# Optimization experiments

Hardware: AMD Instinct MI355X
Metric: run time of the kernel (lower is better)

## Reference

```python
import jax, jax.numpy as jnp
import numpy as np

N = 40000          # spots (nodes)
G = 3000           # genes (input features)
C = 20             # num_classes
E = N * 16         # edges (avg degree 16)


def _uniform(key, shape, stdv):
    return jax.random.uniform(key, shape, jnp.float32, -stdv, stdv)


def _linear_params(key, n_in, n_out):
    # torch Linear default init: U(-1/sqrt(in), 1/sqrt(in)); stored as [in, out]
    k1, k2 = jax.random.split(key)
    s = 1.0 / np.sqrt(n_in)
    return _uniform(k1, (n_in, n_out), s), _uniform(k2, (n_out,), s)


def setup_inputs() -> dict:
    key = jax.random.key(0)
    ks = jax.random.split(key, 32)
    x = jax.random.normal(ks[0], (N, G), jnp.float32)
    adj_rows = jax.random.randint(ks[1], (E,), 0, N, jnp.int32)
    adj_cols = jax.random.randint(ks[2], (E,), 0, N, jnp.int32)
    adj_vals = jax.random.uniform(ks[3], (E,), jnp.float32)

    # GCN weights: GraphConvolution init U(-1/sqrt(out), 1/sqrt(out)), no bias
    def gcn_w(k, fi, fo):
        return _uniform(k, (fi, fo), 1.0 / np.sqrt(fo))

    inp = {
        "x": x, "adj_rows": adj_rows, "adj_cols": adj_cols, "adj_vals": adj_vals,
        "W1": gcn_w(ks[4], G, 512), "W2": gcn_w(ks[5], 512, 256),
        "W3": gcn_w(ks[6], 256, 128), "W4": gcn_w(ks[7], 128, 128),
        "W5": gcn_w(ks[8], 128, C),
    }
    # AE linear layers
    for name, (fi, fo), k in [
        ("enc1", (G, 512), ks[9]), ("enc2", (512, 256), ks[10]),
        ("enc3", (256, 128), ks[11]), ("zl", (128, 128), ks[12]),
        ("dec1", (128, 128), ks[13]), ("dec2", (128, 256), ks[14]),
        ("dec3", (256, 512), ks[15]), ("xbar", (512, G), ks[16]),
    ]:
        w, b = _linear_params(k, fi, fo)
        inp[name + "_w"], inp[name + "_b"] = w, b
    # Attention projection vectors (Linear(in_size, 1, bias=False))
    inp["a1"] = _uniform(ks[17], (512,), 1.0 / np.sqrt(512))
    inp["a2"] = _uniform(ks[18], (256,), 1.0 / np.sqrt(256))
    inp["a3"] = _uniform(ks[19], (128,), 1.0 / np.sqrt(128))
    inp["a4"] = _uniform(ks[20], (128,), 1.0 / np.sqrt(128))
    inp["scale"] = jax.random.normal(ks[21], (G,), jnp.float32)
    inp["additive"] = jax.random.normal(ks[22], (G,), jnp.float32)
    return inp


def _spmm(rows, cols, vals, dense, n):
    # out[r] = sum_e vals[e] * dense[cols[e]] for rows[e]==r  (sparse [n,n] @ dense)
    return jax.ops.segment_sum(vals[:, None] * dense[cols], rows, num_segments=n)


def _gcn(x, rows, cols, vals, W, n, active=True):
    out = _spmm(rows, cols, vals, x @ W, n)
    return jax.nn.relu(out) if active else out


def _attn(h, t, a):
    # stack two [N,D] branches, softmax over the branch axis, weighted sum
    z = jnp.stack([h, t], axis=1)           # [N,2,D]
    w = jnp.einsum('nbd,d->nb', z, a)        # [N,2]
    beta = jax.nn.softmax(w, axis=1)
    return jnp.einsum('nb,nbd->nd', beta, z)


def reference(x, adj_rows, adj_cols, adj_vals,
              W1, W2, W3, W4, W5,
              enc1_w, enc1_b, enc2_w, enc2_b, enc3_w, enc3_b, zl_w, zl_b,
              dec1_w, dec1_b, dec2_w, dec2_b, dec3_w, dec3_b, xbar_w, xbar_b,
              a1, a2, a3, a4, scale, additive):
    n = x.shape[0]
    # autoencoder
    t1 = jax.nn.relu(x @ enc1_w + enc1_b)
    t2 = jax.nn.relu(t1 @ enc2_w + enc2_b)
    t3 = jax.nn.relu(t2 @ enc3_w + enc3_b)
    z = t3 @ zl_w + zl_b
    d1 = jax.nn.relu(z @ dec1_w + dec1_b)
    d2 = jax.nn.relu(d1 @ dec2_w + dec2_b)
    d3 = jax.nn.relu(d2 @ dec3_w + dec3_b)
    x_bar = d3 @ xbar_w + xbar_b
    # GCN stack with attention-fused AE skip connections
    h = _gcn(x, adj_rows, adj_cols, adj_vals, W1, n)
    emb = _attn(h, t1, a1)
    h = _gcn(emb, adj_rows, adj_cols, adj_vals, W2, n)
    emb = _attn(h, t2, a2)
    h = _gcn(emb, adj_rows, adj_cols, adj_vals, W3, n)
    emb = _attn(h, t3, a3)
    h = _gcn(emb, adj_rows, adj_cols, adj_vals, W4, n)
    emb = _attn(h, z, a4)
    output = _gcn(emb, adj_rows, adj_cols, adj_vals, W5, n, active=False)
    return output, x_bar, jax.nn.sigmoid(scale), jnp.exp(additive)
```

## Files before the change

### kernel.cpp

```cpp
#include <hip/hip_runtime.h>
#include <cmath>

typedef unsigned short u16;
typedef unsigned int u32;
typedef __attribute__((ext_vector_type(8))) short short8;
typedef __attribute__((ext_vector_type(4))) short short4v;
typedef __attribute__((ext_vector_type(4))) float f32x4;

__device__ __forceinline__ float bf2f(u16 h) {
  union { u32 u; float f; } v; v.u = ((u32)h) << 16; return v.f;
}
__device__ __forceinline__ u16 f2bf(float f) {
  union { float f; u32 u; } v; v.f = f;
  u32 u = v.u;
  u32 r = (u + 0x7FFFu + ((u >> 16) & 1u)) >> 16;
  return (u16)r;
}

__global__ void convx_kernel(const float* __restrict__ x, u16* __restrict__ A0) {
  int idx = blockIdx.x * 256 + threadIdx.x;
  int r = blockIdx.y;
  if (idx >= 376) return;
  short8 o;
  if (r < 40000 && idx < 375) {
    const float* src = x + (size_t)r * 3000 + idx * 8;
    float4 v0 = *(const float4*)src;
    float4 v1 = *(const float4*)(src + 4);
    o[0] = (short)f2bf(v0.x); o[1] = (short)f2bf(v0.y);
    o[2] = (short)f2bf(v0.z); o[3] = (short)f2bf(v0.w);
    o[4] = (short)f2bf(v1.x); o[5] = (short)f2bf(v1.y);
    o[6] = (short)f2bf(v1.z); o[7] = (short)f2bf(v1.w);
  } else {
#pragma unroll
    for (int j = 0; j < 8; ++j) o[j] = 0;
  }
  *(short8*)(A0 + (size_t)r * 3008 + idx * 8) = o;
}

__global__ void convw_kernel(const float* __restrict__ W, u16* __restrict__ Wt,
                             int K, int N, int Kp) {
  int k = blockIdx.x * 256 + threadIdx.x;
  int n = blockIdx.y;
  if (k >= Kp) return;
  float v = (k < K && n < N) ? W[(size_t)k * N + n] : 0.f;
  Wt[(size_t)n * Kp + k] = f2bf(v);
}

__global__ void zero_kernel(int* p, int n) {
  int i = blockIdx.x * 256 + threadIdx.x;
  if (i < n) p[i] = 0;
}
__global__ void count_kernel(const int* __restrict__ rows, int* __restrict__ counts, int E) {
  int i = blockIdx.x * 256 + threadIdx.x;
  if (i < E) atomicAdd(&counts[rows[i]], 1);
}
__global__ __launch_bounds__(1024) void scan_kernel(const int* __restrict__ counts,
                                                    int* __restrict__ rowptr,
                                                    int* __restrict__ cursor, int n) {
  __shared__ int buf[1024];
  __shared__ int carry_s;
  int tid = threadIdx.x;
  if (tid == 0) carry_s = 0;
  __syncthreads();
  for (int base = 0; base < n; base += 1024) {
    int i = base + tid;
    int v = (i < n) ? counts[i] : 0;
    buf[tid] = v;
    __syncthreads();
    for (int off = 1; off < 1024; off <<= 1) {
      int tv = (tid >= off) ? buf[tid - off] : 0;
      __syncthreads();
      buf[tid] += tv;
      __syncthreads();
    }
    int incl = buf[tid];
    int carry = carry_s;
    if (i < n) { int ex = carry + incl - v; rowptr[i] = ex; cursor[i] = ex; }
    __syncthreads();
    if (tid == 1023) carry_s = carry + incl;
    __syncthreads();
  }
  if (tid == 0) rowptr[n] = carry_s;
}
__global__ void scatter_kernel(const int* __restrict__ rows, const int* __restrict__ cols,
                               const float* __restrict__ vals, int* __restrict__ cursor,
                               int* __restrict__ cols_s, float* __restrict__ vals_s, int E) {
  int i = blockIdx.x * 256 + threadIdx.x;
  if (i < E) {
    int r = rows[i];
    int p = atomicAdd(&cursor[r], 1);
    cols_s[p] = cols[i];
    vals_s[p] = vals[i];
  }
}

#define BM 128
#define BN 128
#define BK 32

template <bool BIAS, bool RELU, bool OUTBF16, int CH>
__global__ __launch_bounds__(256, 2) void gemm_bf16(
    const u16* __restrict__ A, int lda, const u16* __restrict__ Bt, int ldb,
    void* __restrict__ C1, int ldc,
    const float* __restrict__ bias, int M, int Nreal, int K, int MT, int NT) {
  __shared__ __align__(16) u16 As[2][BM * BK];
  __shared__ __align__(16) u16 Bs[2][BN * BK];
  const int lin = blockIdx.x;
  const int per = CH * NT;
  const int g = lin / per;
  const int r0 = lin - g * per;
  const int bx0 = g * CH;
  const int cw = min(CH, MT - bx0);
  const int bx = bx0 + r0 % cw;
  const int by = r0 / cw;

  const int tid = threadIdx.x;
  const int lane = tid & 63;
  const int wave = tid >> 6;
  const int mblk = bx * BM;
  const int nblk = by * BN;
  const int wm = (wave & 1) * 64;
  const int wn = (wave >> 1) * 64;
  const int ml = lane & 15;
  const int kg = lane >> 4;

  f32x4 acc[4][4];
#pragma unroll
  for (int i = 0; i < 4; ++i)
#pragma unroll
    for (int j = 0; j < 4; ++j) acc[i][j] = (f32x4)(0.f);

  const int nk = K / BK;
  const int sr = tid >> 2;
  const int sc = (tid & 3) * 8;
  const u16* gA0 = A + (size_t)(mblk + sr) * lda + sc;
  const u16* gA1 = A + (size_t)(mblk + sr + 64) * lda + sc;
  const u16* gB0 = Bt + (size_t)(nblk + sr) * ldb + sc;
  const u16* gB1 = Bt + (size_t)(nblk + sr + 64) * ldb + sc;

  auto stage = [&](int buf, int kt) {
    const int ko = kt * BK;
    u16* lA = &As[buf][0] + wave * 512;
    u16* lB = &Bs[buf][0] + wave * 512;
    __builtin_amdgcn_global_load_lds((const void*)(gA0 + ko), (void*)lA, 16, 0, 0);
    __builtin_amdgcn_global_load_lds((const void*)(gA1 + ko), (void*)(lA + 2048), 16, 0, 0);
    __builtin_amdgcn_global_load_lds((const void*)(gB0 + ko), (void*)lB, 16, 0, 0);
    __builtin_amdgcn_global_load_lds((const void*)(gB1 + ko), (void*)(lB + 2048), 16, 0, 0);
  };

  stage(0, 0);
  asm volatile("s_waitcnt vmcnt(0)" ::: "memory");
  __syncthreads();

  int cur = 0;
  for (int kt = 0; kt < nk; ++kt) {
    if (kt + 1 < nk) stage(cur ^ 1, kt + 1);
    short8 af[4], bfr[4];
#pragma unroll
    for (int i = 0; i < 4; ++i) {
      af[i] = *(const short8*)&As[cur][(wm + i * 16 + ml) * BK + kg * 8];
      bfr[i] = *(const short8*)&Bs[cur][(wn + i * 16 + ml) * BK + kg * 8];
    }
#pragma unroll
    for (int i = 0; i < 4; ++i)
#pragma unroll
      for (int j = 0; j < 4; ++j)
        acc[i][j] = __builtin_amdgcn_mfma_f32_16x16x32_bf16(af[i], bfr[j], acc[i][j], 0, 0, 0);
    asm volatile("s_waitcnt vmcnt(0)" ::: "memory");
    __syncthreads();
    cur ^= 1;
  }

#pragma unroll
  for (int i = 0; i < 4; ++i) {
    const int row0 = mblk + wm + i * 16 + kg * 4;
#pragma unroll
    for (int j = 0; j < 4; ++j) {
      const int col = nblk + wn + j * 16 + ml;
      if (col < Nreal) {
        float bv = BIAS ? bias[col] : 0.f;
#pragma unroll
        for (int r = 0; r < 4; ++r) {
          const int row = row0 + r;
          if (row < M) {
            float v = acc[i][j][r] + bv;
            if (RELU) v = fmaxf(v, 0.f);
            if (OUTBF16)
              ((u16*)C1)[(size_t)row * ldc + col] = f2bf(v);
            else
              ((float*)C1)[(size_t)row * ldc + col] = v;
          }
        }
      }
    }
  }
}

template <int MODE>
__global__ __launch_bounds__(512, 1) void gemm256p(
    const u16* __restrict__ A, int lda, const u16* __restrict__ Bt, int ldb,
    void* __restrict__ C1, void* __restrict__ C2, int ldc,
    const float* __restrict__ bias, int M, int Nreal, int K, int MT2, int NT) {
  __shared__ __align__(16) u16 smem[2 * 2 * 256 * 64];
  const int tid = threadIdx.x;
  const int lane = tid & 63;
  const int wave = tid >> 6;
  const int wm = wave >> 2;
  const int wn = wave & 3;
  const int ml = lane & 15;
  const int kg = lane >> 4;

  const int grp = blockIdx.x / (8 * NT);
  const int rr = blockIdx.x % (8 * NT);
  const int nb = min(8, MT2 - grp * 8);
  const int bx = grp * 8 + rr % nb;
  const int by = rr / nb;
  const int mblk = bx * 256;
  const int nblk = by * 256;

  f32x4 acc[8][4];
#pragma unroll
  for (int i = 0; i < 8; ++i)
#pragma unroll
    for (int j = 0; j < 4; ++j) acc[i][j] = (f32x4)(0.f);

  const int srow = tid >> 3;
  const int clog = (tid & 7) ^ (srow & 7);
  const size_t abase = (size_t)(mblk + srow) * lda + clog * 8;
  const size_t bbase = (size_t)(nblk + srow) * ldb + clog * 8;
  const int NKT = K / 64;

  auto stageA = [&](int d, int kt, int h) {
    u16* dst = smem + d * 16384 + h * 4096 + wave * 512;
    const u16* src = A + abase + (size_t)h * 64 * lda + kt * 64;
    __builtin_amdgcn_global_load_lds((const void*)src, (void*)dst, 16, 0, 0);
  };
  auto stageB = [&](int d, int kt, int h) {
    u16* dst = smem + 32768 + d * 16384 + h * 4096 + wave * 512;
    const u16* src = Bt + bbase + (size_t)h * 64 * ldb + kt * 64;
    __builtin_amdgcn_global_load_lds((const void*)src, (void*)dst, 16, 0, 0);
  };
  auto stageU0 = [&](int d, int kt) { stageB(d, kt, 0); stageB(d, kt, 1); };
  auto stageU1 = [&](int d, int kt) { stageB(d, kt, 2); stageB(d, kt, 3); };
  auto stageU2 = [&](int d, int kt) { stageA(d, kt, 0); stageA(d, kt, 2); };
  auto stageU3 = [&](int d, int kt) { stageA(d, kt, 1); stageA(d, kt, 3); };
  auto readA = [&](int d, int im, int kk) -> short8 {
    const int r = wm * 128 + im * 16 + ml;
    const int ch = (kk * 4 + kg) ^ (r & 7);
    return *(const short8*)&smem[d * 16384 + r * 64 + ch * 8];
  };
  auto readB = [&](int d, int j, int kk) -> short8 {
    const int r = wn * 64 + j * 16 + ml;
    const int ch = (kk * 4 + kg) ^ (r & 7);
    return *(const short8*)&smem[32768 + d * 16384 + r * 64 + ch * 8];
  };

  stageU0(0, 0); stageU1(0, 0); stageU2(0, 0); stageU3(0, 0);
  asm volatile("s_waitcnt vmcnt(2)" ::: "memory");
  __builtin_amdgcn_s_barrier();

  for (int kt = 0; kt < NKT; ++kt) {
    const int d = kt & 1;
    const bool more = (kt + 1 < NKT);
    short8 b[4][2];
#pragma unroll
    for (int j = 0; j < 4; ++j) { b[j][0] = readB(d, j, 0); b[j][1] = readB(d, j, 1); }
    {
      short8 a00 = readA(d, 0, 0), a01 = readA(d, 0, 1);
      short8 a10 = readA(d, 1, 0), a11 = readA(d, 1, 1);
      if (more) stageU0(d ^ 1, kt + 1);
      __builtin_amdgcn_s_setprio(1);
#pragma unroll
      for (int j = 0; j < 4; ++j) {
        acc[0][j] = __builtin_amdgcn_mfma_f32_16x16x32_bf16(a00, b[j][0], acc[0][j], 0, 0, 0);
        acc[1][j] = __builtin_amdgcn_mfma_f32_16x16x32_bf16(a10, b[j][0], acc[1][j], 0, 0, 0);
      }
#pragma unroll
      for (int j = 0; j < 4; ++j) {
        acc[0][j] = __builtin_amdgcn_mfma_f32_16x16x32_bf16(a01, b[j][1], acc[0][j], 0, 0, 0);
        acc[1][j] = __builtin_amdgcn_mfma_f32_16x16x32_bf16(a11, b[j][1], acc[1][j], 0, 0, 0);
      }
      __builtin_amdgcn_s_setprio(0);
    }
    {
      short8 a00 = readA(d, 2, 0), a01 = readA(d, 2, 1);
      short8 a10 = readA(d, 3, 0), a11 = readA(d, 3, 1);
      if (more) stageU1(d ^ 1, kt + 1);
      __builtin_amdgcn_s_setprio(1);
#pragma unroll
      for (int j = 0; j < 4; ++j) {
        acc[2][j] = __builtin_amdgcn_mfma_f32_16x16x32_bf16(a00, b[j][0], acc[2][j], 0, 0, 0);
        acc[3][j] = __builtin_amdgcn_mfma_f32_16x16x32_bf16(a10, b[j][0], acc[3][j], 0, 0, 0);
      }
#pragma unroll
      for (int j = 0; j < 4; ++j) {
        acc[2][j] = __builtin_amdgcn_mfma_f32_16x16x32_bf16(a01, b[j][1], acc[2][j], 0, 0, 0);
        acc[3][j] = __builtin_amdgcn_mfma_f32_16x16x32_bf16(a11, b[j][1], acc[3][j], 0, 0, 0);
      }
      __builtin_amdgcn_s_setprio(0);
    }
    if (more) asm volatile("s_waitcnt vmcnt(4)" ::: "memory");
    else      asm volatile("s_waitcnt vmcnt(0)" ::: "memory");
    __builtin_amdgcn_s_barrier();
    {
      short8 a00 = readA(d, 4, 0), a01 = readA(d, 4, 1);
      short8 a10 = readA(d, 5, 0), a11 = readA(d, 5, 1);
      if (more) stageU2(d ^ 1, kt + 1);
      __builtin_amdgcn_s_setprio(1);
#pragma unroll
      for (int j = 0; j < 4; ++j) {
        acc[4][j] = __builtin_amdgcn_mfma_f32_16x16x32_bf16(a00, b[j][0], acc[4][j], 0, 0, 0);
        acc[5][j] = __builtin_amdgcn_mfma_f32_16x16x32_bf16(a10, b[j][0], acc[5][j], 0, 0, 0);
      }
#pragma unroll
      for (int j = 0; j < 4; ++j) {
        acc[4][j] = __builtin_amdgcn_mfma_f32_16x16x32_bf16(a01, b[j][1], acc[4][j], 0, 0, 0);
        acc[5][j] = __builtin_amdgcn_mfma_f32_16x16x32_bf16(a11, b[j][1], acc[5][j], 0, 0, 0);
      }
      __builtin_amdgcn_s_setprio(0);
    }
    {
      short8 a00 = readA(d, 6, 0), a01 = readA(d, 6, 1);
      short8 a10 = readA(d, 7, 0), a11 = readA(d, 7, 1);
      if (more) stageU3(d ^ 1, kt + 1);
      __builtin_amdgcn_s_setprio(1);
#pragma unroll
      for (int j = 0; j < 4; ++j) {
        acc[6][j] = __builtin_amdgcn_mfma_f32_16x16x32_bf16(a00, b[j][0], acc[6][j], 0, 0, 0);
        acc[7][j] = __builtin_amdgcn_mfma_f32_16x16x32_bf16(a10, b[j][0], acc[7][j], 0, 0, 0);
      }
#pragma unroll
      for (int j = 0; j < 4; ++j) {
        acc[6][j] = __builtin_amdgcn_mfma_f32_16x16x32_bf16(a01, b[j][1], acc[6][j], 0, 0, 0);
        acc[7][j] = __builtin_amdgcn_mfma_f32_16x16x32_bf16(a11, b[j][1], acc[7][j], 0, 0, 0);
      }
      __builtin_amdgcn_s_setprio(0);
    }
    if (more) asm volatile("s_waitcnt vmcnt(2)" ::: "memory");
    __builtin_amdgcn_s_barrier();
  }

  __syncthreads();

  float* ep = (float*)smem;
  const int ES = 260;
  const int colg = nblk + lane * 4;
  const bool second = (MODE == 0) && (nblk >= 512);
  float bv0 = 0.f, bv1 = 0.f, bv2 = 0.f, bv3 = 0.f;
  if (MODE == 0) {
    if (!second) { float4 b4 = *(const float4*)(bias + colg); bv0 = b4.x; bv1 = b4.y; bv2 = b4.z; bv3 = b4.w; }
  } else {
    if (colg + 3 < Nreal) {
      float4 b4 = *(const float4*)(bias + colg);
      bv0 = b4.x; bv1 = b4.y; bv2 = b4.z; bv3 = b4.w;
    } else {
      if (colg + 0 < Nreal) bv0 = bias[colg + 0];
      if (colg + 1 < Nreal) bv1 = bias[colg + 1];
      if (colg + 2 < Nreal) bv2 = bias[colg + 2];
      if (colg + 3 < Nreal) bv3 = bias[colg + 3];
    }
  }
#pragma unroll
  for (int p = 0; p < 4; ++p) {
    if (p) __syncthreads();
    if (wm == (p >> 1)) {
#pragma unroll
      for (int ii = 0; ii < 4; ++ii) {
        const int i = (p & 1) * 4 + ii;
        const int lrow0 = ii * 16 + kg * 4;
#pragma unroll
        for (int j = 0; j < 4; ++j) {
          const int colL = wn * 64 + j * 16 + ml;
#pragma unroll
          for (int r = 0; r < 4; ++r) ep[(lrow0 + r) * ES + colL] = acc[i][j][r];
        }
      }
    }
    __syncthreads();
#pragma unroll
    for (int it = 0; it < 8; ++it) {
      const int lrow = wave * 8 + it;
      const int grow = mblk + p * 64 + lrow;
      if (grow < M) {
        float v0 = ep[lrow * ES + lane * 4 + 0] + bv0;
        float v1 = ep[lrow * ES + lane * 4 + 1] + bv1;
        float v2 = ep[lrow * ES + lane * 4 + 2] + bv2;
        float v3 = ep[lrow * ES + lane * 4 + 3] + bv3;
        if (MODE == 0) {
          if (!second) { v0 = fmaxf(v0, 0.f); v1 = fmaxf(v1, 0.f); v2 = fmaxf(v2, 0.f); v3 = fmaxf(v3, 0.f); }
          u16* dst = (second ? (u16*)C2 : (u16*)C1) + (size_t)grow * 512 + (second ? colg - 512 : colg);
          short4v o;
          o[0] = (short)f2bf(v0); o[1] = (short)f2bf(v1);
          o[2] = (short)f2bf(v2); o[3] = (short)f2bf(v3);
          *(short4v*)dst = o;
        } else {
          float* dst = (float*)C1 + (size_t)grow * ldc + colg;
          if (colg + 3 < Nreal) {
            float4 v; v.x = v0; v.y = v1; v.z = v2; v.w = v3;
            *(float4*)dst = v;
          } else {
            if (colg + 0 < Nreal) dst[0] = v0;
            if (colg + 1 < Nreal) dst[1] = v1;
            if (colg + 2 < Nreal) dst[2] = v2;
            if (colg + 3 < Nreal) dst[3] = v3;
          }
        }
      }
    }
  }
}

template <int D>
__global__ __launch_bounds__(256) void spmm_attn(const int* __restrict__ rowptr,
                                                 const int* __restrict__ colidx,
                                                 const float* __restrict__ vals,
                                                 const u16* __restrict__ X,
                                                 const u16* __restrict__ T,
                                                 const float* __restrict__ a,
                                                 u16* __restrict__ emb) {
  constexpr int VE = D / 64;
  const int wave = threadIdx.x >> 6, lane = threadIdx.x & 63;
  const int row = blockIdx.x * 4 + wave;
  const int co = lane * VE;
  float h[VE];
#pragma unroll
  for (int j = 0; j < VE; ++j) h[j] = 0.f;
  const int s = rowptr[row], e = rowptr[row + 1];
  for (int base = s; base < e; base += 64) {
    const int n = min(64, e - base);
    int myc = 0; float myv = 0.f;
    if (base + lane < e) { myc = colidx[base + lane]; myv = vals[base + lane]; }
    for (int jj = 0; jj < n; ++jj) {
      const int c = __shfl(myc, jj);
      const float v = __shfl(myv, jj);
      const u16* xr = X + (size_t)c * D + co;
      if constexpr (VE == 8) {
        short8 x8 = *(const short8*)xr;
#pragma unroll
        for (int j = 0; j < 8; ++j) h[j] += v * bf2f((u16)x8[j]);
      } else if constexpr (VE == 4) {
        short4v x4 = *(const short4v*)xr;
#pragma unroll
        for (int j = 0; j < 4; ++j) h[j] += v * bf2f((u16)x4[j]);
      } else {
        u32 x2 = *(const u32*)xr;
        h[0] += v * bf2f((u16)(x2 & 0xffffu));
        h[1] += v * bf2f((u16)(x2 >> 16));
      }
    }
  }
#pragma unroll
  for (int j = 0; j < VE; ++j) h[j] = fmaxf(h[j], 0.f);

  float tv[VE];
  const u16* tr = T + (size_t)row * D + co;
  if constexpr (VE == 8) {
    short8 t8 = *(const short8*)tr;
#pragma unroll
    for (int j = 0; j < 8; ++j) tv[j] = bf2f((u16)t8[j]);
  } else if constexpr (VE == 4) {
    short4v t4 = *(const short4v*)tr;
#pragma unroll
    for (int j = 0; j < 4; ++j) tv[j] = bf2f((u16)t4[j]);
  } else {
    u32 t2 = *(const u32*)tr;
    tv[0] = bf2f((u16)(t2 & 0xffffu)); tv[1] = bf2f((u16)(t2 >> 16));
  }

  float wh = 0.f, wt = 0.f;
#pragma unroll
  for (int j = 0; j < VE; ++j) {
    float av = a[co + j];
    wh += av * h[j];
    wt += av * tv[j];
  }
  for (int off = 32; off; off >>= 1) {
    wh += __shfl_xor(wh, off);
    wt += __shfl_xor(wt, off);
  }
  float m = fmaxf(wh, wt);
  float e1 = expf(wh - m), e2 = expf(wt - m);
  float inv = 1.f / (e1 + e2);
  float b1 = e1 * inv, b2 = e2 * inv;
  u16* er = emb + (size_t)row * D + co;
  if constexpr (VE == 8) {
    short8 o;
#pragma unroll
    for (int j = 0; j < 8; ++j) o[j] = (short)f2bf(b1 * h[j] + b2 * tv[j]);
    *(short8*)er = o;
  } else if constexpr (VE == 4) {
    short4v o;
#pragma unroll
    for (int j = 0; j < 4; ++j) o[j] = (short)f2bf(b1 * h[j] + b2 * tv[j]);
    *(short4v*)er = o;
  } else {
    *(u32*)er = (u32)f2bf(b1 * h[0] + b2 * tv[0]) | ((u32)f2bf(b1 * h[1] + b2 * tv[1]) << 16);
  }
}

#define XROWS 12
__global__ __launch_bounds__(256) void xw5_blk(const u16* __restrict__ emb,
                                               const float* __restrict__ W5,
                                               u16* __restrict__ xw5, int Nrow) {
  __shared__ float W5s[128 * 20];
  __shared__ u16 embs[XROWS * 128];
  const int tid = threadIdx.x;
  const int row0 = blockIdx.x * XROWS;
  for (int i = tid; i < 2560; i += 256) W5s[i] = W5[i];
  if (tid < 192) {
    const int base = tid * 8;
    const int grow = row0 + base / 128;
    short8 v;
    if (grow < Nrow) v = *(const short8*)(emb + (size_t)row0 * 128 + base);
    else {
#pragma unroll
      for (int j = 0; j < 8; ++j) v[j] = 0;
    }
    *(short8*)(embs + base) = v;
  }
  __syncthreads();
  const int r = tid / 20;
  const int c = tid % 20;
  if (r < XROWS && tid < 240) {
    const int grow = row0 + r;
    if (grow < Nrow) {
      float acc = 0.f;
#pragma unroll 8
      for (int k = 0; k < 128; ++k) acc += bf2f(embs[r * 128 + k]) * W5s[k * 20 + c];
      xw5[(size_t)grow * 20 + c] = f2bf(acc);
    }
  }
}

__global__ __launch_bounds__(256) void spmm_out_blk(const int* __restrict__ rowptr,
                                                    const int* __restrict__ colidx,
                                                    const float* __restrict__ vals,
                                                    const u16* __restrict__ X,
                                                    float* __restrict__ Y, int Nrow) {
  const int tid = threadIdx.x;
  const int r = tid / 20;
  const int c = tid % 20;
  if (r >= XROWS || tid >= 240) return;
  const int row = blockIdx.x * XROWS + r;
  if (row >= Nrow) return;
  float acc = 0.f;
  const int s = rowptr[row], e = rowptr[row + 1];
  for (int i = s; i < e; ++i) {
    const int col = colidx[i];
    acc += vals[i] * bf2f(X[(size_t)col * 20 + c]);
  }
  Y[(size_t)row * 20 + c] = acc;
}

__global__ void sig_exp_kernel(const float* __restrict__ scale, const float* __restrict__ additive,
                               float* __restrict__ osig, float* __restrict__ oexp, int g) {
  int i = blockIdx.x * 256 + threadIdx.x;
  if (i < g) {
    osig[i] = 1.f / (1.f + expf(-scale[i]));
    oexp[i] = expf(additive[i]);
  }
}

extern "C" void kernel_launch(void* const* d_in, const int* in_sizes, int n_in,
                              void* d_out, int out_size, void* d_ws, size_t ws_size,
                              hipStream_t stream) {
  (void)n_in; (void)out_size; (void)ws_size;
  const float* x      = (const float*)d_in[0];
  const int*   arows  = (const int*)d_in[1];
  const int*   acols  = (const int*)d_in[2];
  const float* avals  = (const float*)d_in[3];
  const float* W1     = (const float*)d_in[4];
  const float* W2     = (const float*)d_in[5];
  const float* W3     = (const float*)d_in[6];
  const float* W4     = (const float*)d_in[7];
  const float* W5     = (const float*)d_in[8];
  const float* enc1_w = (const float*)d_in[9],  *enc1_b = (const float*)d_in[10];
  const float* enc2_w = (const float*)d_in[11], *enc2_b = (const float*)d_in[12];
  const float* enc3_w = (const float*)d_in[13], *enc3_b = (const float*)d_in[14];
  const float* zl_w   = (const float*)d_in[15], *zl_b   = (const float*)d_in[16];
  const float* dec1_w = (const float*)d_in[17], *dec1_b = (const float*)d_in[18];
  const float* dec2_w = (const float*)d_in[19], *dec2_b = (const float*)d_in[20];
  const float* dec3_w = (const float*)d_in[21], *dec3_b = (const float*)d_in[22];
  const float* xbar_w = (const float*)d_in[23], *xbar_b = (const float*)d_in[24];
  const float* a1 = (const float*)d_in[25], *a2 = (const float*)d_in[26];
  const float* a3 = (const float*)d_in[27], *a4 = (const float*)d_in[28];
  const float* scale = (const float*)d_in[29], *additive = (const float*)d_in[30];

  const int E = in_sizes[1];
  const int N = 40000, G = 3000, Kx = 3008;
  const int Mp = 40192;

  float* out      = (float*)d_out;
  float* out_gcn  = out;
  float* out_xbar = out + (size_t)N * 20;
  float* out_sig  = out_xbar + (size_t)N * G;
  float* out_exp  = out_sig + G;

  char* wsb = (char*)d_ws;
  size_t off = 0;
  auto alloc = [&](size_t b) -> void* {
    void* p = wsb + off;
    off = (off + b + 255) & ~(size_t)255;
    return p;
  };
  u16* A0    = (u16*)alloc((size_t)Mp * Kx * 2);
  u16* t1    = (u16*)alloc((size_t)Mp * 512 * 2);
  u16* t2    = (u16*)alloc((size_t)Mp * 256 * 2);
  u16* t3    = (u16*)alloc((size_t)Mp * 128 * 2);
  u16* zb    = (u16*)alloc((size_t)Mp * 128 * 2);
  u16* dd1   = (u16*)alloc((size_t)Mp * 128 * 2);
  u16* dd2   = (u16*)alloc((size_t)Mp * 256 * 2);
  u16* dd3   = (u16*)alloc((size_t)Mp * 512 * 2);
  u16* xw    = (u16*)alloc((size_t)Mp * 512 * 2);
  u16* emb   = (u16*)alloc((size_t)Mp * 512 * 2);
  u16* xw5   = (u16*)alloc((size_t)N * 20 * 2);
  u16* catT  = (u16*)alloc((size_t)1024 * Kx * 2);
  u16* enc2T = (u16*)alloc((size_t)256 * 512 * 2);
  u16* enc3T = (u16*)alloc((size_t)128 * 256 * 2);
  u16* zlT   = (u16*)alloc((size_t)128 * 128 * 2);
  u16* dec1T = (u16*)alloc((size_t)128 * 128 * 2);
  u16* dec2T = (u16*)alloc((size_t)256 * 128 * 2);
  u16* dec3T = (u16*)alloc((size_t)512 * 256 * 2);
  u16* xbarT = (u16*)alloc((size_t)3072 * 512 * 2);
  u16* W2T   = (u16*)alloc((size_t)256 * 512 * 2);
  u16* W3T   = (u16*)alloc((size_t)128 * 256 * 2);
  u16* W4T   = (u16*)alloc((size_t)128 * 128 * 2);
  int* counts = (int*)alloc((size_t)N * 4);
  int* rowptr = (int*)alloc((size_t)(N + 1) * 4);
  int* cursor = (int*)alloc((size_t)N * 4);
  int* colss  = (int*)alloc((size_t)E * 4);
  float* valss = (float*)alloc((size_t)E * 4);

  convx_kernel<<<dim3(2, Mp), 256, 0, stream>>>(x, A0);
  auto convw = [&](const float* W, u16* Wt, int K, int Nw, int Kp, int Np) {
    convw_kernel<<<dim3((Kp + 255) / 256, Np), 256, 0, stream>>>(W, Wt, K, Nw, Kp);
  };
  convw(enc1_w, catT,             3000, 512, Kx, 512);
  convw(W1,     catT + 512 * Kx,  3000, 512, Kx, 512);
  convw(enc2_w, enc2T, 512, 256, 512, 256);
  convw(enc3_w, enc3T, 256, 128, 256, 128);
  convw(zl_w,   zlT,   128, 128, 128, 128);
  convw(dec1_w, dec1T, 128, 128, 128, 128);
  convw(dec2_w, dec2T, 128, 256, 128, 256);
  convw(dec3_w, dec3T, 256, 512, 256, 512);
  convw(xbar_w, xbarT, 512, 3000, 512, 3072);
  convw(W2,     W2T,   512, 256, 512, 256);
  convw(W3,     W3T,   256, 128, 256, 128);
  convw(W4,     W4T,   128, 128, 128, 128);

  zero_kernel<<<(N + 255) / 256, 256, 0, stream>>>(counts, N);
  count_kernel<<<(E + 255) / 256, 256, 0, stream>>>(arows, counts, E);
  scan_kernel<<<1, 1024, 0, stream>>>(counts, rowptr, cursor, N);
  scatter_kernel<<<(E + 255) / 256, 256, 0, stream>>>(arows, acols, avals, cursor, colss, valss, E);

  const int MT = 313;
  const int MT2 = 157;
  gemm256p<0><<<MT2 * 4, 512, 0, stream>>>(
      A0, Kx, catT, Kx, t1, xw, 512, enc1_b, N, 1024, Kx, MT2, 4);
  gemm_bf16<true, true, true, 32><<<MT * 2, 256, 0, stream>>>(
      t1, 512, enc2T, 512, t2, 256, enc2_b, N, 256, 512, MT, 2);
  gemm_bf16<true, true, true, 32><<<MT * 1, 256, 0, stream>>>(
      t2, 256, enc3T, 256, t3, 128, enc3_b, N, 128, 256, MT, 1);
  gemm_bf16<true, false, true, 32><<<MT * 1, 256, 0, stream>>>(
      t3, 128, zlT, 128, zb, 128, zl_b, N, 128, 128, MT, 1);
  gemm_bf16<true, true, true, 32><<<MT * 1, 256, 0, stream>>>(
      zb, 128, dec1T, 128, dd1, 128, dec1_b, N, 128, 128, MT, 1);
  gemm_bf16<true, true, true, 32><<<MT * 2, 256, 0, stream>>>(
      dd1, 128, dec2T, 128, dd2, 256, dec2_b, N, 256, 128, MT, 2);
  gemm_bf16<true, true, true, 32><<<MT * 4, 256, 0, stream>>>(
      dd2, 256, dec3T, 256, dd3, 512, dec3_b, N, 512, 256, MT, 4);
  gemm256p<1><<<MT2 * 12, 512, 0, stream>>>(
      dd3, 512, xbarT, 512, out_xbar, nullptr, 3000, xbar_b, N, 3000, 512, MT2, 12);

  spmm_attn<512><<<N / 4, 256, 0, stream>>>(rowptr, colss, valss, xw, t1, a1, emb);
  gemm_bf16<false, false, true, 32><<<MT * 2, 256, 0, stream>>>(
      emb, 512, W2T, 512, xw, 256, nullptr, N, 256, 512, MT, 2);
  spmm_attn<256><<<N / 4, 256, 0, stream>>>(rowptr, colss, valss, xw, t2, a2, emb);
  gemm_bf16<false, false, true, 32><<<MT * 1, 256, 0, stream>>>(
      emb, 256, W3T, 256, xw, 128, nullptr, N, 128, 256, MT, 1);
  spmm_attn<128><<<N / 4, 256, 0, stream>>>(rowptr, colss, valss, xw, t3, a3, emb);
  gemm_bf16<false, false, true, 32><<<MT * 1, 256, 0, stream>>>(
      emb, 128, W4T, 128, xw, 128, nullptr, N, 128, 128, MT, 1);
  spmm_attn<128><<<N / 4, 256, 0, stream>>>(rowptr, colss, valss, xw, zb, a4, emb);

  const int XB = (N + XROWS - 1) / XROWS;
  xw5_blk<<<XB, 256, 0, stream>>>(emb, W5, xw5, N);
  spmm_out_blk<<<XB, 256, 0, stream>>>(rowptr, colss, valss, xw5, out_gcn, N);

  sig_exp_kernel<<<(G + 255) / 256, 256, 0, stream>>>(scale, additive, out_sig, out_exp, G);
}
```

Measured before the change: 1.288 ms.

## Fuse fp32-to-bf16 conversion of x into the first GEMM's A-tile load

Removes the separate convx pass that converted x to a padded bf16 buffer. The MODE 0 GEMM now loads fp32 rows of x into registers, converts them to bf16 and writes them swizzled into LDS, prefetching the next k-tile while the MFMAs run. This drops one full write and re-read of a 40000x3008 bf16 intermediate. In exchange the kernel reads fp32 (twice the bytes) once per N-tile (4 tiles), uses more registers, and replaces the async global-to-LDS path with manual stores.

Result: slower. 1.383 ms (+7.4%).

```diff
diff --git a/kernel.cpp b/kernel.cpp
--- a/kernel.cpp
+++ b/kernel.cpp
@@ -15,26 +15,6 @@
   u32 u = v.u;
   u32 r = (u + 0x7FFFu + ((u >> 16) & 1u)) >> 16;
   return (u16)r;
-}
-
-__global__ void convx_kernel(const float* __restrict__ x, u16* __restrict__ A0) {
-  int idx = blockIdx.x * 256 + threadIdx.x;
-  int r = blockIdx.y;
-  if (idx >= 376) return;
-  short8 o;
-  if (r < 40000 && idx < 375) {
-    const float* src = x + (size_t)r * 3000 + idx * 8;
-    float4 v0 = *(const float4*)src;
-    float4 v1 = *(const float4*)(src + 4);
-    o[0] = (short)f2bf(v0.x); o[1] = (short)f2bf(v0.y);
-    o[2] = (short)f2bf(v0.z); o[3] = (short)f2bf(v0.w);
-    o[4] = (short)f2bf(v1.x); o[5] = (short)f2bf(v1.y);
-    o[6] = (short)f2bf(v1.z); o[7] = (short)f2bf(v1.w);
-  } else {
-#pragma unroll
-    for (int j = 0; j < 8; ++j) o[j] = 0;
-  }
-  *(short8*)(A0 + (size_t)r * 3008 + idx * 8) = o;
 }
 
 __global__ void convw_kernel(const float* __restrict__ W, u16* __restrict__ Wt,
@@ -226,15 +206,9 @@
 
   const int srow = tid >> 3;
   const int clog = (tid & 7) ^ (srow & 7);
-  const size_t abase = (size_t)(mblk + srow) * lda + clog * 8;
   const size_t bbase = (size_t)(nblk + srow) * ldb + clog * 8;
   const int NKT = K / 64;
 
-  auto stageA = [&](int d, int kt, int h) {
-    u16* dst = smem + d * 16384 + h * 4096 + wave * 512;
-    const u16* src = A + abase + (size_t)h * 64 * lda + kt * 64;
-    __builtin_amdgcn_global_load_lds((const void*)src, (void*)dst, 16, 0, 0);
-  };
   auto stageB = [&](int d, int kt, int h) {
     u16* dst = smem + 32768 + d * 16384 + h * 4096 + wave * 512;
     const u16* src = Bt + bbase + (size_t)h * 64 * ldb + kt * 64;
@@ -242,8 +216,6 @@
   };
   auto stageU0 = [&](int d, int kt) { stageB(d, kt, 0); stageB(d, kt, 1); };
   auto stageU1 = [&](int d, int kt) { stageB(d, kt, 2); stageB(d, kt, 3); };
-  auto stageU2 = [&](int d, int kt) { stageA(d, kt, 0); stageA(d, kt, 2); };
-  auto stageU3 = [&](int d, int kt) { stageA(d, kt, 1); stageA(d, kt, 3); };
   auto readA = [&](int d, int im, int kk) -> short8 {
     const int r = wm * 128 + im * 16 + ml;
     const int ch = (kk * 4 + kg) ^ (r & 7);
@@ -255,89 +227,191 @@
     return *(const short8*)&smem[32768 + d * 16384 + r * 64 + ch * 8];
   };
 
-  stageU0(0, 0); stageU1(0, 0); stageU2(0, 0); stageU3(0, 0);
-  asm volatile("s_waitcnt vmcnt(2)" ::: "memory");
-  __builtin_amdgcn_s_barrier();
-
-  for (int kt = 0; kt < NKT; ++kt) {
-    const int d = kt & 1;
-    const bool more = (kt + 1 < NKT);
-    short8 b[4][2];
-#pragma unroll
-    for (int j = 0; j < 4; ++j) { b[j][0] = readB(d, j, 0); b[j][1] = readB(d, j, 1); }
-    {
-      short8 a00 = readA(d, 0, 0), a01 = readA(d, 0, 1);
-      short8 a10 = readA(d, 1, 0), a11 = readA(d, 1, 1);
-      if (more) stageU0(d ^ 1, kt + 1);
-      __builtin_amdgcn_s_setprio(1);
+  if constexpr (MODE == 0) {
+    const float* X = (const float*)A;
+    const int arow = tid >> 1;
+    const int ahalf = tid & 1;
+    const int growA = mblk + arow;
+    const bool rowok = growA < M;
+    const float* xrow = X + (size_t)growA * lda;
+    float4 a4[8];
+
+    auto issueA = [&](int kt) {
+      const int k0 = kt * 64 + ahalf * 32;
+      if (rowok && k0 + 32 <= lda) {
+#pragma unroll
+        for (int j = 0; j < 8; ++j) a4[j] = *(const float4*)(xrow + k0 + j * 4);
+      } else {
+#pragma unroll
+        for (int j = 0; j < 8; ++j) {
+          float e0 = 0.f, e1 = 0.f, e2 = 0.f, e3 = 0.f;
+          if (rowok) {
+            const int kc = k0 + j * 4;
+            if (kc + 0 < lda) e0 = xrow[kc + 0];
+            if (kc + 1 < lda) e1 = xrow[kc + 1];
+            if (kc + 2 < lda) e2 = xrow[kc + 2];
+            if (kc + 3 < lda) e3 = xrow[kc + 3];
+          }
+          float4 t; t.x = e0; t.y = e1; t.z = e2; t.w = e3;
+          a4[j] = t;
+        }
+      }
+    };
+    auto writeA = [&](int d) {
 #pragma unroll
       for (int j = 0; j < 4; ++j) {
-        acc[0][j] = __builtin_amdgcn_mfma_f32_16x16x32_bf16(a00, b[j][0], acc[0][j], 0, 0, 0);
-        acc[1][j] = __builtin_amdgcn_mfma_f32_16x16x32_bf16(a10, b[j][0], acc[1][j], 0, 0, 0);
-      }
-#pragma unroll
-      for (int j = 0; j < 4; ++j) {
-        acc[0][j] = __builtin_amdgcn_mfma_f32_16x16x32_bf16(a01, b[j][1], acc[0][j], 0, 0, 0);
-        acc[1][j] = __builtin_amdgcn_mfma_f32_16x16x32_bf16(a11, b[j][1], acc[1][j], 0, 0, 0);
-      }
-      __builtin_amdgcn_s_setprio(0);
-    }
-    {
-      short8 a00 = readA(d, 2, 0), a01 = readA(d, 2, 1);
-      short8 a10 = readA(d, 3, 0), a11 = readA(d, 3, 1);
-      if (more) stageU1(d ^ 1, kt + 1);
-      __builtin_amdgcn_s_setprio(1);
-#pragma unroll
-      for (int j = 0; j < 4; ++j) {
-        acc[2][j] = __builtin_amdgcn_mfma_f32_16x16x32_bf16(a00, b[j][0], acc[2][j], 0, 0, 0);
-        acc[3][j] = __builtin_amdgcn_mfma_f32_16x16x32_bf16(a10, b[j][0], acc[3][j], 0, 0, 0);
-      }
-#pragma unroll
-      for (int j = 0; j < 4; ++j) {
-        acc[2][j] = __builtin_amdgcn_mfma_f32_16x16x32_bf16(a01, b[j][1], acc[2][j], 0, 0, 0);
-        acc[3][j] = __builtin_amdgcn_mfma_f32_16x16x32_bf16(a11, b[j][1], acc[3][j], 0, 0, 0);
-      }
-      __builtin_amdgcn_s_setprio(0);
-    }
-    if (more) asm volatile("s_waitcnt vmcnt(4)" ::: "memory");
-    else      asm volatile("s_waitcnt vmcnt(0)" ::: "memory");
+        float4 lo = a4[2 * j], hi = a4[2 * j + 1];
+        short8 v;
+        v[0] = (short)f2bf(lo.x); v[1] = (short)f2bf(lo.y);
+        v[2] = (short)f2bf(lo.z); v[3] = (short)f2bf(lo.w);
+        v[4] = (short)f2bf(hi.x); v[5] = (short)f2bf(hi.y);
+        v[6] = (short)f2bf(hi.z); v[7] = (short)f2bf(hi.w);
+        const int ch = (ahalf * 4 + j) ^ (arow & 7);
+        *(short8*)&smem[d * 16384 + arow * 64 + ch * 8] = v;
+      }
+    };
+
+    issueA(0);
+    stageU0(0, 0); stageU1(0, 0);
+    asm volatile("s_waitcnt vmcnt(4)" ::: "memory");
+    writeA(0);
+    __syncthreads();
+
+    for (int kt = 0; kt < NKT; ++kt) {
+      const int d = kt & 1;
+      const bool more = (kt + 1 < NKT);
+      short8 b[4][2];
+#pragma unroll
+      for (int j = 0; j < 4; ++j) { b[j][0] = readB(d, j, 0); b[j][1] = readB(d, j, 1); }
+      short8 aC0k0 = readA(d, 0, 0), aC0k1 = readA(d, 0, 1);
+      short8 aC1k0 = readA(d, 1, 0), aC1k1 = readA(d, 1, 1);
+      if (more) {
+        issueA(kt + 1);
+        stageU0(d ^ 1, kt + 1);
+        stageU1(d ^ 1, kt + 1);
+      }
+#pragma unroll
+      for (int q = 0; q < 4; ++q) {
+        short8 aN0k0, aN0k1, aN1k0, aN1k1;
+        if (q < 3) {
+          aN0k0 = readA(d, 2 * (q + 1), 0);     aN0k1 = readA(d, 2 * (q + 1), 1);
+          aN1k0 = readA(d, 2 * (q + 1) + 1, 0); aN1k1 = readA(d, 2 * (q + 1) + 1, 1);
+        }
+        __builtin_amdgcn_s_setprio(1);
+#pragma unroll
+        for (int j = 0; j < 4; ++j) {
+          acc[2 * q][j]     = __builtin_amdgcn_mfma_f32_16x16x32_bf16(aC0k0, b[j][0], acc[2 * q][j], 0, 0, 0);
+          acc[2 * q + 1][j] = __builtin_amdgcn_mfma_f32_16x16x32_bf16(aC1k0, b[j][0], acc[2 * q + 1][j], 0, 0, 0);
+        }
+#pragma unroll
+        for (int j = 0; j < 4; ++j) {
+          acc[2 * q][j]     = __builtin_amdgcn_mfma_f32_16x16x32_bf16(aC0k1, b[j][1], acc[2 * q][j], 0, 0, 0);
+          acc[2 * q + 1][j] = __builtin_amdgcn_mfma_f32_16x16x32_bf16(aC1k1, b[j][1], acc[2 * q + 1][j], 0, 0, 0);
+        }
+        __builtin_amdgcn_s_setprio(0);
+        if (q < 3) { aC0k0 = aN0k0; aC0k1 = aN0k1; aC1k0 = aN1k0; aC1k1 = aN1k1; }
+      }
+      if (more) {
+        asm volatile("s_waitcnt vmcnt(4)" ::: "memory");
+        writeA(d ^ 1);
+      }
+      asm volatile("s_waitcnt vmcnt(0) lgkmcnt(0)" ::: "memory");
+      __builtin_amdgcn_s_barrier();
+    }
+  } else {
+    const size_t abase = (size_t)(mblk + srow) * lda + clog * 8;
+    auto stageA = [&](int d, int kt, int h) {
+      u16* dst = smem + d * 16384 + h * 4096 + wave * 512;
+      const u16* src = A + abase + (size_t)h * 64 * lda + kt * 64;
+      __builtin_amdgcn_global_load_lds((const void*)src, (void*)dst, 16, 0, 0);
+    };
+    auto stageU2 = [&](int d, int kt) { stageA(d, kt, 0); stageA(d, kt, 2); };
+    auto stageU3 = [&](int d, int kt) { stageA(d, kt, 1); stageA(d, kt, 3); };
+
+    stageU0(0, 0); stageU1(0, 0); stageU2(0, 0); stageU3(0, 0);
+    asm volatile("s_waitcnt vmcnt(2)" ::: "memory");
     __builtin_amdgcn_s_barrier();
-    {
-      short8 a00 = readA(d, 4, 0), a01 = readA(d, 4, 1);
-      short8 a10 = readA(d, 5, 0), a11 = readA(d, 5, 1);
-      if (more) stageU2(d ^ 1, kt + 1);
-      __builtin_amdgcn_s_setprio(1);
-#pragma unroll
-      for (int j = 0; j < 4; ++j) {
-        acc[4][j] = __builtin_amdgcn_mfma_f32_16x16x32_bf16(a00, b[j][0], acc[4][j], 0, 0, 0);
-        acc[5][j] = __builtin_amdgcn_mfma_f32_16x16x32_bf16(a10, b[j][0], acc[5][j], 0, 0, 0);
-      }
-#pragma unroll
-      for (int j = 0; j < 4; ++j) {
-        acc[4][j] = __builtin_amdgcn_mfma_f32_16x16x32_bf16(a01, b[j][1], acc[4][j], 0, 0, 0);
-        acc[5][j] = __builtin_amdgcn_mfma_f32_16x16x32_bf16(a11, b[j][1], acc[5][j], 0, 0, 0);
-      }
-      __builtin_amdgcn_s_setprio(0);
-    }
-    {
-      short8 a00 = readA(d, 6, 0), a01 = readA(d, 6, 1);
-      short8 a10 = readA(d, 7, 0), a11 = readA(d, 7, 1);
-      if (more) stageU3(d ^ 1, kt + 1);
-      __builtin_amdgcn_s_setprio(1);
-#pragma unroll
-      for (int j = 0; j < 4; ++j) {
-        acc[6][j] = __builtin_amdgcn_mfma_f32_16x16x32_bf16(a00, b[j][0], acc[6][j], 0, 0, 0);
-        acc[7][j] = __builtin_amdgcn_mfma_f32_16x16x32_bf16(a10, b[j][0], acc[7][j], 0, 0, 0);
-      }
-#pragma unroll
-      for (int j = 0; j < 4; ++j) {
-        acc[6][j] = __builtin_amdgcn_mfma_f32_16x16x32_bf16(a01, b[j][1], acc[6][j], 0, 0, 0);
-        acc[7][j] = __builtin_amdgcn_mfma_f32_16x16x32_bf16(a11, b[j][1], acc[7][j], 0, 0, 0);
-      }
-      __builtin_amdgcn_s_setprio(0);
-    }
-    if (more) asm volatile("s_waitcnt vmcnt(2)" ::: "memory");
-    __builtin_amdgcn_s_barrier();
+
+    for (int kt = 0; kt < NKT; ++kt) {
+      const int d = kt & 1;
+      const bool more = (kt + 1 < NKT);
+      short8 b[4][2];
+#pragma unroll
+      for (int j = 0; j < 4; ++j) { b[j][0] = readB(d, j, 0); b[j][1] = readB(d, j, 1); }
+      {
+        short8 a00 = readA(d, 0, 0), a01 = readA(d, 0, 1);
+        short8 a10 = readA(d, 1, 0), a11 = readA(d, 1, 1);
+        if (more) stageU0(d ^ 1, kt + 1);
+        __builtin_amdgcn_s_setprio(1);
+#pragma unroll
+        for (int j = 0; j < 4; ++j) {
+          acc[0][j] = __builtin_amdgcn_mfma_f32_16x16x32_bf16(a00, b[j][0], acc[0][j], 0, 0, 0);
+          acc[1][j] = __builtin_amdgcn_mfma_f32_16x16x32_bf16(a10, b[j][0], acc[1][j], 0, 0, 0);
+        }
+#pragma unroll
+        for (int j = 0; j < 4; ++j) {
+          acc[0][j] = __builtin_amdgcn_mfma_f32_16x16x32_bf16(a01, b[j][1], acc[0][j], 0, 0, 0);
+          acc[1][j] = __builtin_amdgcn_mfma_f32_16x16x32_bf16(a11, b[j][1], acc[1][j], 0, 0, 0);
+        }
+        __builtin_amdgcn_s_setprio(0);
+      }
+      {
+        short8 a00 = readA(d, 2, 0), a01 = readA(d, 2, 1);
+        short8 a10 = readA(d, 3, 0), a11 = readA(d, 3, 1);
+        if (more) stageU1(d ^ 1, kt + 1);
+        __builtin_amdgcn_s_setprio(1);
+#pragma unroll
+        for (int j = 0; j < 4; ++j) {
+          acc[2][j] = __builtin_amdgcn_mfma_f32_16x16x32_bf16(a00, b[j][0], acc[2][j], 0, 0, 0);
+          acc[3][j] = __builtin_amdgcn_mfma_f32_16x16x32_bf16(a10, b[j][0], acc[3][j], 0, 0, 0);
+        }
+#pragma unroll
+        for (int j = 0; j < 4; ++j) {
+          acc[2][j] = __builtin_amdgcn_mfma_f32_16x16x32_bf16(a01, b[j][1], acc[2][j], 0, 0, 0);
+          acc[3][j] = __builtin_amdgcn_mfma_f32_16x16x32_bf16(a11, b[j][1], acc[3][j], 0, 0, 0);
+        }
+        __builtin_amdgcn_s_setprio(0);
+      }
+      if (more) asm volatile("s_waitcnt vmcnt(4)" ::: "memory");
+      else      asm volatile("s_waitcnt vmcnt(0)" ::: "memory");
+      __builtin_amdgcn_s_barrier();
+      {
+        short8 a00 = readA(d, 4, 0), a01 = readA(d, 4, 1);
+        short8 a10 = readA(d, 5, 0), a11 = readA(d, 5, 1);
+        if (more) stageU2(d ^ 1, kt + 1);
+        __builtin_amdgcn_s_setprio(1);
+#pragma unroll
+        for (int j = 0; j < 4; ++j) {
+          acc[4][j] = __builtin_amdgcn_mfma_f32_16x16x32_bf16(a00, b[j][0], acc[4][j], 0, 0, 0);
+          acc[5][j] = __builtin_amdgcn_mfma_f32_16x16x32_bf16(a10, b[j][0], acc[5][j], 0, 0, 0);
+        }
+#pragma unroll
+        for (int j = 0; j < 4; ++j) {
+          acc[4][j] = __builtin_amdgcn_mfma_f32_16x16x32_bf16(a01, b[j][1], acc[4][j], 0, 0, 0);
+          acc[5][j] = __builtin_amdgcn_mfma_f32_16x16x32_bf16(a11, b[j][1], acc[5][j], 0, 0, 0);
+        }
+        __builtin_amdgcn_s_setprio(0);
+      }
+      {
+        short8 a00 = readA(d, 6, 0), a01 = readA(d, 6, 1);
+        short8 a10 = readA(d, 7, 0), a11 = readA(d, 7, 1);
+        if (more) stageU3(d ^ 1, kt + 1);
+        __builtin_amdgcn_s_setprio(1);
+#pragma unroll
+        for (int j = 0; j < 4; ++j) {
+          acc[6][j] = __builtin_amdgcn_mfma_f32_16x16x32_bf16(a00, b[j][0], acc[6][j], 0, 0, 0);
+          acc[7][j] = __builtin_amdgcn_mfma_f32_16x16x32_bf16(a10, b[j][0], acc[7][j], 0, 0, 0);
+        }
+#pragma unroll
+        for (int j = 0; j < 4; ++j) {
+          acc[6][j] = __builtin_amdgcn_mfma_f32_16x16x32_bf16(a01, b[j][1], acc[6][j], 0, 0, 0);
+          acc[7][j] = __builtin_amdgcn_mfma_f32_16x16x32_bf16(a11, b[j][1], acc[7][j], 0, 0, 0);
+        }
+        __builtin_amdgcn_s_setprio(0);
+      }
+      if (more) asm volatile("s_waitcnt vmcnt(2)" ::: "memory");
+      __builtin_amdgcn_s_barrier();
+    }
   }
 
   __syncthreads();
@@ -603,7 +677,6 @@
     off = (off + b + 255) & ~(size_t)255;
     return p;
   };
-  u16* A0    = (u16*)alloc((size_t)Mp * Kx * 2);
   u16* t1    = (u16*)alloc((size_t)Mp * 512 * 2);
   u16* t2    = (u16*)alloc((size_t)Mp * 256 * 2);
   u16* t3    = (u16*)alloc((size_t)Mp * 128 * 2);
@@ -631,7 +704,6 @@
   int* colss  = (int*)alloc((size_t)E * 4);
   float* valss = (float*)alloc((size_t)E * 4);
 
-  convx_kernel<<<dim3(2, Mp), 256, 0, stream>>>(x, A0);
   auto convw = [&](const float* W, u16* Wt, int K, int Nw, int Kp, int Np) {
     convw_kernel<<<dim3((Kp + 255) / 256, Np), 256, 0, stream>>>(W, Wt, K, Nw, Kp);
   };
@@ -656,7 +728,7 @@
   const int MT = 313;
   const int MT2 = 157;
   gemm256p<0><<<MT2 * 4, 512, 0, stream>>>(
-      A0, Kx, catT, Kx, t1, xw, 512, enc1_b, N, 1024, Kx, MT2, 4);
+      (const u16*)x, 3000, catT, Kx, t1, xw, 512, enc1_b, N, 1024, Kx, MT2, 4);
   gemm_bf16<true, true, true, 32><<<MT * 2, 256, 0, stream>>>(
       t1, 512, enc2T, 512, t2, 256, enc2_b, N, 256, 512, MT, 2);
   gemm_bf16<true, true, true, 32><<<MT * 1, 256, 0, stream>>>(
```
